# Performance work log

Measured on AMD Instinct MI355X. Metric: run time of the kernel, lower is better.

## Reference

```python
import jax, jax.numpy as jnp
import numpy as np

B, H, S, D = 2, 16, 2048, 64


def setup_inputs() -> dict:
    key = jax.random.key(0)
    kq, kk, kv = jax.random.split(key, 3)
    Q = jax.random.normal(kq, (B, H, S, D), dtype=jnp.float32)
    K = jax.random.normal(kk, (B, H, S, D), dtype=jnp.float32)
    V = jax.random.normal(kv, (B, H, S, D), dtype=jnp.float32)
    return {
        "Q": Q,
        "K": K,
        "V": V,
        "is_causal": 1,
        "softmax_scale": jnp.float32(1.0 / np.sqrt(D)),
    }


def reference(Q, K, V, is_causal, softmax_scale):
    seq_len = Q.shape[2]
    # [B, H, S, S] materialized scores, as in the original module
    scores = jnp.einsum("bhqd,bhkd->bhqk", Q, K) * softmax_scale
    if is_causal:
        causal = jnp.tril(jnp.ones((seq_len, seq_len), dtype=bool))
        scores = jnp.where(causal, scores, -jnp.inf)
    P = jax.nn.softmax(scores.astype(jnp.float32), axis=-1)
    out = jnp.einsum("bhqk,bhkd->bhqd", P, V)
    return out
```

## Files before the change

kernel.cpp:

```cpp
#include <hip/hip_runtime.h>
#include <stdint.h>

#define S_  2048
#define D_  64
#define KP  68
#define NT  (S_/64)
#define BH  32

typedef __bf16 bf16x8 __attribute__((ext_vector_type(8)));
typedef float  f32x4  __attribute__((ext_vector_type(4)));

__global__ __launch_bounds__(512, 6) void fattn_kernel(
    const float* __restrict__ Q,
    const float* __restrict__ K,
    const float* __restrict__ V,
    const int* __restrict__ causal_p,
    const float* __restrict__ scale_p,
    float* __restrict__ O)
{
  __shared__ __bf16 Klds[64 * KP];
  __shared__ __bf16 Vlds[2][64 * KP];
  __shared__ __bf16 Plds[8][16 * KP];

  const int tid  = threadIdx.x;
  const int w    = tid >> 6;
  const int lane = tid & 63;
  const int quad = lane >> 4;
  const int n    = lane & 15;
  const int strip = w >> 1;
  const int h     = w & 1;

  const int bid  = blockIdx.x;
  const int bh   = bid & 31;
  const int tq   = NT - 1 - (bid >> 5);
  const long base = (long)bh * S_ * D_;
  const int causal  = *causal_p;
  const float qs = (*scale_p) * 1.44269504f;

  const int krow = tid >> 3;
  const int kc8  = tid & 7;
  const int vk   = tid & 63;
  const int vc8  = tid >> 6;

  float4 pka, pkb, pva, pvb;

  auto issueLoads = [&](int kt) {
    const float* kp = K + base + (long)(kt + krow) * D_ + kc8 * 8;
    pka = *(const float4*)(kp);
    pkb = *(const float4*)(kp + 4);
    const float* vp = V + base + (long)(kt + vk) * D_ + vc8 * 8;
    pva = *(const float4*)(vp);
    pvb = *(const float4*)(vp + 4);
  };
  auto stageK = [&]() {
    bf16x8 kv;
    kv[0] = (__bf16)pka.x; kv[1] = (__bf16)pka.y; kv[2] = (__bf16)pka.z; kv[3] = (__bf16)pka.w;
    kv[4] = (__bf16)pkb.x; kv[5] = (__bf16)pkb.y; kv[6] = (__bf16)pkb.z; kv[7] = (__bf16)pkb.w;
    *(bf16x8*)(&Klds[krow * KP + kc8 * 8]) = kv;
  };
  auto stageV = [&](int buf) {
    float vv[8] = {pva.x, pva.y, pva.z, pva.w, pvb.x, pvb.y, pvb.z, pvb.w};
#pragma unroll
    for (int j = 0; j < 8; j++)
      Vlds[buf][(vc8 * 8 + j) * KP + vk] = (__bf16)vv[j];
  };

  float* Osc = (float*)&Plds[0][0];
  float* Lsc = Osc + 4 * 16 * 65;

  const int q0  = tq * 64;
  const int lim = causal ? tq : (NT - 1);

  bf16x8 qf[2];
  {
    const float* qp = Q + base + (long)(q0 + strip * 16 + n) * D_;
#pragma unroll
    for (int kk = 0; kk < 2; kk++) {
      float4 a = *(const float4*)(qp + kk * 32 + quad * 8);
      float4 b = *(const float4*)(qp + kk * 32 + quad * 8 + 4);
      qf[kk][0] = (__bf16)(a.x * qs); qf[kk][1] = (__bf16)(a.y * qs);
      qf[kk][2] = (__bf16)(a.z * qs); qf[kk][3] = (__bf16)(a.w * qs);
      qf[kk][4] = (__bf16)(b.x * qs); qf[kk][5] = (__bf16)(b.y * qs);
      qf[kk][6] = (__bf16)(b.z * qs); qf[kk][7] = (__bf16)(b.w * qs);
    }
  }

  f32x4 oacc[4];
  float lpart[4];
#pragma unroll
  for (int t = 0; t < 4; t++) oacc[t] = (f32x4){0.f, 0.f, 0.f, 0.f};
#pragma unroll
  for (int r = 0; r < 4; r++) lpart[r] = 0.f;

  issueLoads(0);
  stageK();
  stageV(0);
  __syncthreads();

  for (int kt2 = 0; kt2 <= lim; ++kt2) {
    const int curV = kt2 & 1;
    const bool haveNext = (kt2 < lim);
    if (haveNext) issueLoads((kt2 + 1) * 64);
    const bool diag = causal && (kt2 == tq);

#pragma unroll
    for (int t = 0; t < 2; t++) {
      f32x4 c = (f32x4){0.f, 0.f, 0.f, 0.f};
#pragma unroll
      for (int kk = 0; kk < 2; kk++) {
        bf16x8 bfrag = *(const bf16x8*)(&Klds[(h * 32 + t * 16 + n) * KP + kk * 32 + quad * 8]);
        c = __builtin_amdgcn_mfma_f32_16x16x32_bf16(qf[kk], bfrag, c, 0, 0, 0);
      }
      if (!diag) {
#pragma unroll
        for (int r = 0; r < 4; r++) {
          float p = __builtin_exp2f(c[r]);
          lpart[r] += p;
          Plds[w][(quad * 4 + r) * KP + t * 16 + n] = (__bf16)p;
        }
      } else {
        const int kg = kt2 * 64 + h * 32 + t * 16 + n;
#pragma unroll
        for (int r = 0; r < 4; r++) {
          int qg = q0 + strip * 16 + quad * 4 + r;
          float p = (kg > qg) ? 0.0f : __builtin_exp2f(c[r]);
          lpart[r] += p;
          Plds[w][(quad * 4 + r) * KP + t * 16 + n] = (__bf16)p;
        }
      }
    }

    __syncthreads();

    {
      bf16x8 pf = *(const bf16x8*)(&Plds[w][n * KP + quad * 8]);
#pragma unroll
      for (int td = 0; td < 4; td++) {
        bf16x8 vfrag = *(const bf16x8*)(&Vlds[curV][(td * 16 + n) * KP + h * 32 + quad * 8]);
        oacc[td] = __builtin_amdgcn_mfma_f32_16x16x32_bf16(pf, vfrag, oacc[td], 0, 0, 0);
      }
    }
    if (haveNext) { stageK(); stageV(curV ^ 1); }
    __syncthreads();
  }

#pragma unroll
  for (int r = 0; r < 4; r++) {
#pragma unroll
    for (int off = 1; off < 16; off <<= 1)
      lpart[r] += __shfl_xor(lpart[r], off, 64);
  }
  if (h == 1) {
#pragma unroll
    for (int td = 0; td < 4; td++)
#pragma unroll
      for (int r = 0; r < 4; r++)
        Osc[(strip * 16 + quad * 4 + r) * 65 + td * 16 + n] = oacc[td][r];
    if (n == 0) {
#pragma unroll
      for (int r = 0; r < 4; r++) Lsc[strip * 16 + quad * 4 + r] = lpart[r];
    }
  }
  __syncthreads();
  if (h == 0) {
    float linv[4];
#pragma unroll
    for (int r = 0; r < 4; r++)
      linv[r] = 1.0f / (lpart[r] + Lsc[strip * 16 + quad * 4 + r]);
#pragma unroll
    for (int td = 0; td < 4; td++) {
#pragma unroll
      for (int r = 0; r < 4; r++) {
        float o = (oacc[td][r] + Osc[(strip * 16 + quad * 4 + r) * 65 + td * 16 + n]) * linv[r];
        O[base + (long)(q0 + strip * 16 + quad * 4 + r) * D_ + td * 16 + n] = o;
      }
    }
  }
}

extern "C" void kernel_launch(void* const* d_in, const int* in_sizes, int n_in,
                              void* d_out, int out_size, void* d_ws, size_t ws_size,
                              hipStream_t stream) {
  (void)in_sizes; (void)n_in; (void)d_ws; (void)ws_size; (void)out_size;
  const float* Q = (const float*)d_in[0];
  const float* K = (const float*)d_in[1];
  const float* V = (const float*)d_in[2];
  const int*   causal_p = (const int*)d_in[3];
  const float* scale_p  = (const float*)d_in[4];
  float* O = (float*)d_out;

  fattn_kernel<<<dim3(NT * BH), 512, 0, stream>>>(Q, K, V, causal_p, scale_p, O);
}
```

Measured before the change: 142.0 us.

## Transpose QK MFMA so P stays wave-local; double-buffer K and drop one barrier per tile

Swaps the MFMA operands for QK^T so each lane holds a column of scores, which lets it write P as one 4-wide bf16 store into a per-wave buffer. The P->PV handoff then needs no block barrier, and the row sum reduces with two shuffles instead of four. K is now double-buffered like V, so staging the next tile needs only one __syncthreads per iteration instead of two. V loads become coalesced scalar column reads and are written transposed as vector stores. The cost is extra LDS for the second K buffer, which may lower occupancy, and the kernel relies on intra-wave ordering of the P buffer.

```diff
diff --git a/kernel.cpp b/kernel.cpp
--- a/kernel.cpp
+++ b/kernel.cpp
@@ -4,11 +4,15 @@
 #define S_  2048
 #define D_  64
 #define KP  68
+#define PW  40
 #define NT  (S_/64)
 #define BH  32
 
 typedef __bf16 bf16x8 __attribute__((ext_vector_type(8)));
+typedef __bf16 bf16x4 __attribute__((ext_vector_type(4)));
 typedef float  f32x4  __attribute__((ext_vector_type(4)));
+
+#define KVBYTES (64 * KP * 2)
 
 __global__ __launch_bounds__(512, 6) void fattn_kernel(
     const float* __restrict__ Q,
@@ -18,9 +22,9 @@
     const float* __restrict__ scale_p,
     float* __restrict__ O)
 {
-  __shared__ __bf16 Klds[64 * KP];
-  __shared__ __bf16 Vlds[2][64 * KP];
-  __shared__ __bf16 Plds[8][16 * KP];
+  __shared__ __align__(16) char smem[4 * KVBYTES + 8 * 16 * PW * 2];
+  __bf16* const Kbase = (__bf16*)smem;
+  __bf16* const Vbase = (__bf16*)(smem + 2 * KVBYTES);
 
   const int tid  = threadIdx.x;
   const int w    = tid >> 6;
@@ -29,6 +33,8 @@
   const int n    = lane & 15;
   const int strip = w >> 1;
   const int h     = w & 1;
+
+  __bf16* const Pw = (__bf16*)(smem + 4 * KVBYTES) + w * 16 * PW;
 
   const int bid  = blockIdx.x;
   const int bh   = bid & 31;
@@ -39,34 +45,35 @@
 
   const int krow = tid >> 3;
   const int kc8  = tid & 7;
-  const int vk   = tid & 63;
-  const int vc8  = tid >> 6;
 
-  float4 pka, pkb, pva, pvb;
+  float4 pka, pkb;
+  float  pvv[8];
 
   auto issueLoads = [&](int kt) {
     const float* kp = K + base + (long)(kt + krow) * D_ + kc8 * 8;
     pka = *(const float4*)(kp);
     pkb = *(const float4*)(kp + 4);
-    const float* vp = V + base + (long)(kt + vk) * D_ + vc8 * 8;
-    pva = *(const float4*)(vp);
-    pvb = *(const float4*)(vp + 4);
+    const float* vp = V + base + (long)(kt + w * 8) * D_ + lane;
+#pragma unroll
+    for (int j = 0; j < 8; j++) pvv[j] = vp[j * D_];
   };
-  auto stageK = [&]() {
+  auto stageK = [&](int buf) {
     bf16x8 kv;
     kv[0] = (__bf16)pka.x; kv[1] = (__bf16)pka.y; kv[2] = (__bf16)pka.z; kv[3] = (__bf16)pka.w;
     kv[4] = (__bf16)pkb.x; kv[5] = (__bf16)pkb.y; kv[6] = (__bf16)pkb.z; kv[7] = (__bf16)pkb.w;
-    *(bf16x8*)(&Klds[krow * KP + kc8 * 8]) = kv;
+    *(bf16x8*)(&Kbase[buf * 64 * KP + krow * KP + kc8 * 8]) = kv;
   };
   auto stageV = [&](int buf) {
-    float vv[8] = {pva.x, pva.y, pva.z, pva.w, pvb.x, pvb.y, pvb.z, pvb.w};
-#pragma unroll
-    for (int j = 0; j < 8; j++)
-      Vlds[buf][(vc8 * 8 + j) * KP + vk] = (__bf16)vv[j];
+    bf16x4 lo4, hi4;
+    lo4[0] = (__bf16)pvv[0]; lo4[1] = (__bf16)pvv[1]; lo4[2] = (__bf16)pvv[2]; lo4[3] = (__bf16)pvv[3];
+    hi4[0] = (__bf16)pvv[4]; hi4[1] = (__bf16)pvv[5]; hi4[2] = (__bf16)pvv[6]; hi4[3] = (__bf16)pvv[7];
+    __bf16* vd = &Vbase[buf * 64 * KP + lane * KP + w * 8];
+    *(bf16x4*)(vd)     = lo4;
+    *(bf16x4*)(vd + 4) = hi4;
   };
 
-  float* Osc = (float*)&Plds[0][0];
-  float* Lsc = Osc + 4 * 16 * 65;
+  float* Osc = (float*)smem;
+  float* Lh  = Osc + 64 * 65;
 
   const int q0  = tq * 64;
   const int lim = causal ? tq : (NT - 1);
@@ -86,87 +93,86 @@
   }
 
   f32x4 oacc[4];
-  float lpart[4];
+  float lsum = 0.f;
 #pragma unroll
   for (int t = 0; t < 4; t++) oacc[t] = (f32x4){0.f, 0.f, 0.f, 0.f};
-#pragma unroll
-  for (int r = 0; r < 4; r++) lpart[r] = 0.f;
+
+  const int qg = q0 + strip * 16 + n;
 
   issueLoads(0);
-  stageK();
+  stageK(0);
   stageV(0);
   __syncthreads();
 
+  int cur = 0;
   for (int kt2 = 0; kt2 <= lim; ++kt2) {
-    const int curV = kt2 & 1;
     const bool haveNext = (kt2 < lim);
     if (haveNext) issueLoads((kt2 + 1) * 64);
     const bool diag = causal && (kt2 == tq);
+
+    const __bf16* Kc = Kbase + cur * 64 * KP;
+    const __bf16* Vc = Vbase + cur * 64 * KP;
 
 #pragma unroll
     for (int t = 0; t < 2; t++) {
       f32x4 c = (f32x4){0.f, 0.f, 0.f, 0.f};
 #pragma unroll
       for (int kk = 0; kk < 2; kk++) {
-        bf16x8 bfrag = *(const bf16x8*)(&Klds[(h * 32 + t * 16 + n) * KP + kk * 32 + quad * 8]);
-        c = __builtin_amdgcn_mfma_f32_16x16x32_bf16(qf[kk], bfrag, c, 0, 0, 0);
+        bf16x8 bfrag = *(const bf16x8*)(&Kc[(h * 32 + t * 16 + n) * KP + kk * 32 + quad * 8]);
+        c = __builtin_amdgcn_mfma_f32_16x16x32_bf16(bfrag, qf[kk], c, 0, 0, 0);
       }
+      bf16x4 pq;
       if (!diag) {
 #pragma unroll
         for (int r = 0; r < 4; r++) {
           float p = __builtin_exp2f(c[r]);
-          lpart[r] += p;
-          Plds[w][(quad * 4 + r) * KP + t * 16 + n] = (__bf16)p;
+          lsum += p;
+          pq[r] = (__bf16)p;
         }
       } else {
-        const int kg = kt2 * 64 + h * 32 + t * 16 + n;
 #pragma unroll
         for (int r = 0; r < 4; r++) {
-          int qg = q0 + strip * 16 + quad * 4 + r;
+          int kg = kt2 * 64 + h * 32 + t * 16 + quad * 4 + r;
           float p = (kg > qg) ? 0.0f : __builtin_exp2f(c[r]);
-          lpart[r] += p;
-          Plds[w][(quad * 4 + r) * KP + t * 16 + n] = (__bf16)p;
+          lsum += p;
+          pq[r] = (__bf16)p;
         }
+      }
+      *(bf16x4*)(&Pw[n * PW + t * 16 + quad * 4]) = pq;
+    }
+
+    {
+      bf16x8 pf = *(const bf16x8*)(&Pw[n * PW + quad * 8]);
+#pragma unroll
+      for (int td = 0; td < 4; td++) {
+        bf16x8 vfrag = *(const bf16x8*)(&Vc[(td * 16 + n) * KP + h * 32 + quad * 8]);
+        oacc[td] = __builtin_amdgcn_mfma_f32_16x16x32_bf16(pf, vfrag, oacc[td], 0, 0, 0);
       }
     }
 
+    if (haveNext) { stageK(cur ^ 1); stageV(cur ^ 1); }
     __syncthreads();
-
-    {
-      bf16x8 pf = *(const bf16x8*)(&Plds[w][n * KP + quad * 8]);
-#pragma unroll
-      for (int td = 0; td < 4; td++) {
-        bf16x8 vfrag = *(const bf16x8*)(&Vlds[curV][(td * 16 + n) * KP + h * 32 + quad * 8]);
-        oacc[td] = __builtin_amdgcn_mfma_f32_16x16x32_bf16(pf, vfrag, oacc[td], 0, 0, 0);
-      }
-    }
-    if (haveNext) { stageK(); stageV(curV ^ 1); }
-    __syncthreads();
+    cur ^= 1;
   }
 
-#pragma unroll
-  for (int r = 0; r < 4; r++) {
-#pragma unroll
-    for (int off = 1; off < 16; off <<= 1)
-      lpart[r] += __shfl_xor(lpart[r], off, 64);
-  }
+  lsum += __shfl_xor(lsum, 16, 64);
+  lsum += __shfl_xor(lsum, 32, 64);
+  if (quad == 0) Lh[h * 64 + strip * 16 + n] = lsum;
   if (h == 1) {
 #pragma unroll
     for (int td = 0; td < 4; td++)
 #pragma unroll
       for (int r = 0; r < 4; r++)
         Osc[(strip * 16 + quad * 4 + r) * 65 + td * 16 + n] = oacc[td][r];
-    if (n == 0) {
-#pragma unroll
-      for (int r = 0; r < 4; r++) Lsc[strip * 16 + quad * 4 + r] = lpart[r];
-    }
   }
   __syncthreads();
   if (h == 0) {
     float linv[4];
 #pragma unroll
-    for (int r = 0; r < 4; r++)
-      linv[r] = 1.0f / (lpart[r] + Lsc[strip * 16 + quad * 4 + r]);
+    for (int r = 0; r < 4; r++) {
+      int qrow = strip * 16 + quad * 4 + r;
+      linv[r] = 1.0f / (Lh[qrow] + Lh[64 + qrow]);
+    }
 #pragma unroll
     for (int td = 0; td < 4; td++) {
 #pragma unroll
```

After: 231.2 us. +62.8%, slower.
